# Kernel optimization log

Hardware: AMD Instinct MI355X
Metric: run time of the kernel (lower is better)

Reference implementation:

```python
import jax, jax.numpy as jnp
import numpy as np

N_NODES = 20000
N_EDGES = 640000
IN_DIM, HID_DIM, OUT_DIM = 128, 128, 64


def setup_inputs() -> dict:
    key = jax.random.key(0)
    k = jax.random.split(key, 6)
    x = jax.random.normal(k[0], (N_NODES, IN_DIM), dtype=jnp.float32)
    edge_index = jax.random.randint(k[1], (2, N_EDGES), 0, N_NODES, dtype=jnp.int64)
    W1 = jax.random.normal(k[2], (IN_DIM, HID_DIM), dtype=jnp.float32) * (1.0 / np.sqrt(IN_DIM))
    b1 = jnp.zeros((HID_DIM,), dtype=jnp.float32)
    W2 = jax.random.normal(k[3], (HID_DIM, OUT_DIM), dtype=jnp.float32) * (1.0 / np.sqrt(HID_DIM))
    b2 = jnp.zeros((OUT_DIM,), dtype=jnp.float32)
    return {"x": x, "edge_index": edge_index, "W1": W1, "b1": b1, "W2": W2, "b2": b2}


def _gcn_conv(h, W, b, src, dst, n_nodes):
    # h' = D^-1/2 (A + I) D^-1/2 (h W) + b   (PyG GCNConv with self-loops)
    h = h @ W                                              # [N, F_out]
    ones = jnp.ones((src.shape[0],), dtype=h.dtype)
    deg = jax.ops.segment_sum(ones, dst, num_segments=n_nodes) + 1.0  # +1 for self-loop
    dinv = jax.lax.rsqrt(deg)                              # [N]
    w = dinv[src] * dinv[dst]                              # per-edge norm [E]
    msg = h[src] * w[:, None]                              # gather + scale [E, F_out]
    agg = jax.ops.segment_sum(msg, dst, num_segments=n_nodes)  # scatter-add [N, F_out]
    # self-loop contribution: norm_ii = dinv[i]^2
    return agg + h * (dinv * dinv)[:, None] + b


def reference(x, edge_index, W1, b1, W2, b2):
    src, dst = edge_index[0], edge_index[1]
    n = x.shape[0]
    h = _gcn_conv(x, W1, b1, src, dst, n)
    h = jax.nn.relu(h)
    # dropout is identity in eval mode (training=False)
    out = _gcn_conv(h, W2, b2, src, dst, n)
    return out
```

## Files before the change

kernel.cpp:

```cpp
#include <hip/hip_runtime.h>


#define N_NODES 20000
#define N_EDGES 640000
#define IN_DIM 128
#define HID_DIM 128
#define OUT_DIM 64

#define STRIDE 80
#define NRANGE 8
#define RANGE_SZ (N_NODES / NRANGE)
#define SCAT_NB 2048
#define CHUNKS (SCAT_NB / NRANGE)
#define EPC (N_EDGES / CHUNKS)
#define G1_NB 625
#define G1_TASKS (2 * (N_NODES / 16))
#define PRE_ITEMS (128 * 128 + 64 * 128 + N_NODES)
#define PRE_NB ((PRE_ITEMS + 255) / 256)

typedef _Float16 half8_t __attribute__((ext_vector_type(8)));
typedef float float4_t __attribute__((ext_vector_type(4)));

__global__ __launch_bounds__(256) void k_pre(const float* __restrict__ W1,
                                             const float* __restrict__ W2,
                                             _Float16* __restrict__ WT1,
                                             _Float16* __restrict__ WT2,
                                             int* __restrict__ cnt) {
    int i = blockIdx.x * 256 + threadIdx.x;
    if (i < 128 * 128) {
        int c = i >> 7, k = i & 127;
        WT1[i] = (_Float16)W1[k * 128 + c];
    } else if (i < 128 * 128 + 64 * 128) {
        int o = i - 128 * 128;
        int c = o >> 7, k = o & 127;
        WT2[o] = (_Float16)W2[k * 64 + c];
    } else {
        int n = i - (128 * 128 + 64 * 128);
        if (n < N_NODES) cnt[n] = 0;
    }
}

__global__ __launch_bounds__(256) void k_front(const int* __restrict__ src,
                                               const int* __restrict__ dst,
                                               int* __restrict__ cnt,
                                               unsigned short* __restrict__ esrc_pad,
                                               const _Float16* __restrict__ WT1,
                                               const float* __restrict__ x,
                                               _Float16* __restrict__ GA,
                                               _Float16* __restrict__ GB) {
    const int b = blockIdx.x, tid = threadIdx.x;
    if (b < SCAT_NB) {
        const int g = b & 7;
        const int lo = g * RANGE_SZ;
        const int e0 = (b >> 3) * EPC;
        for (int i = tid; i < EPC; i += 256) {
            const int e = e0 + i;
            const int d = __builtin_nontemporal_load(&dst[e]);
            if ((unsigned int)(d - lo) < (unsigned int)RANGE_SZ) {
                const int s = __builtin_nontemporal_load(&src[e]);
                unsigned int rank = atomicAdd((unsigned int*)&cnt[d], 1u);
                if (rank < STRIDE) esrc_pad[d * STRIDE + rank] = (unsigned short)s;
            }
        }
        return;
    }
    const int wave = tid >> 6;
    const int lane = tid & 63;
    const int task = (b - SCAT_NB) * 4 + wave;
    if (task >= G1_TASKS) return;
    const int strip = task >> 1;
    const int nh = task & 1;
    const int row0 = strip * 16;
    const int mrow = row0 + (lane & 15);
    const int kq = (lane >> 4) * 8;
    _Float16* G = nh ? GB : GA;

    half8_t af[4];
#pragma unroll
    for (int kc = 0; kc < 4; ++kc) {
        const float* ap = x + (size_t)mrow * 128 + kc * 32 + kq;
        float4_t f0 = __builtin_nontemporal_load((const float4_t*)ap);
        float4_t f1 = __builtin_nontemporal_load((const float4_t*)(ap + 4));
        half8_t h;
        h[0] = (_Float16)f0[0]; h[1] = (_Float16)f0[1];
        h[2] = (_Float16)f0[2]; h[3] = (_Float16)f0[3];
        h[4] = (_Float16)f1[0]; h[5] = (_Float16)f1[1];
        h[6] = (_Float16)f1[2]; h[7] = (_Float16)f1[3];
        af[kc] = h;
    }
    float4_t acc[4];
#pragma unroll
    for (int nt = 0; nt < 4; ++nt) acc[nt] = (float4_t)(0.0f);
#pragma unroll
    for (int nt = 0; nt < 4; ++nt) {
        const _Float16* wp = WT1 + (size_t)((nh * 4 + nt) * 16 + (lane & 15)) * 128 + kq;
#pragma unroll
        for (int kc = 0; kc < 4; ++kc) {
            half8_t bf = *(const half8_t*)(wp + kc * 32);
            acc[nt] = __builtin_amdgcn_mfma_f32_16x16x32_f16(af[kc], bf, acc[nt], 0, 0, 0);
        }
    }
#pragma unroll
    for (int r = 0; r < 4; ++r) {
        int row = row0 + (lane >> 4) * 4 + r;
#pragma unroll
        for (int nt = 0; nt < 4; ++nt)
            G[(size_t)row * 64 + nt * 16 + (lane & 15)] = (_Float16)acc[nt][r];
    }
}

__global__ __launch_bounds__(256) void k_mid(const int* __restrict__ cnt,
                                             const unsigned short* __restrict__ esrc_pad,
                                             const _Float16* __restrict__ GA,
                                             const _Float16* __restrict__ GB,
                                             const _Float16* __restrict__ WT2,
                                             const float* __restrict__ b1,
                                             _Float16* __restrict__ g2) {
    __shared__ _Float16 h1[16][136];
    const int tid = threadIdx.x;
    const int wave = tid >> 6;
    const int lane = tid & 63;
    const int row0 = blockIdx.x * 16;
    const int eidx = lane >> 3;
    const int fl = lane & 7;

    for (int h = 0; h < 2; ++h) {
        const _Float16* __restrict__ G = h ? GB : GA;
        for (int r4 = 0; r4 < 4; ++r4) {
            const int rr = wave * 4 + r4;
            const int node = row0 + rr;
            const int endt = cnt[node];
            const float dvd = rsqrtf((float)endt + 1.0f);
            const int end = endt < STRIDE ? endt : STRIDE;
            const int base = node * STRIDE;

            float acc[8];
#pragma unroll
            for (int p = 0; p < 8; ++p) acc[p] = 0.0f;
            if (lane < 8) {
                half8_t sv = *(const half8_t*)(G + (size_t)node * 64 + fl * 8);
#pragma unroll
                for (int p = 0; p < 8; ++p) acc[p] = dvd * (float)sv[p];
            }
            int j = 0;
            for (; j + 15 < end; j += 16) {
                int s0 = (int)__builtin_nontemporal_load(&esrc_pad[base + j + eidx]);
                int s1 = (int)__builtin_nontemporal_load(&esrc_pad[base + j + 8 + eidx]);
                float dv0 = rsqrtf((float)cnt[s0] + 1.0f);
                float dv1 = rsqrtf((float)cnt[s1] + 1.0f);
                half8_t r0 = *(const half8_t*)(G + (size_t)s0 * 64 + fl * 8);
                half8_t r1 = *(const half8_t*)(G + (size_t)s1 * 64 + fl * 8);
#pragma unroll
                for (int p = 0; p < 8; ++p)
                    acc[p] += dv0 * (float)r0[p] + dv1 * (float)r1[p];
            }
            for (; j + 7 < end; j += 8) {
                int s = (int)__builtin_nontemporal_load(&esrc_pad[base + j + eidx]);
                float dvs = rsqrtf((float)cnt[s] + 1.0f);
                half8_t r = *(const half8_t*)(G + (size_t)s * 64 + fl * 8);
#pragma unroll
                for (int p = 0; p < 8; ++p) acc[p] += dvs * (float)r[p];
            }
            if (j < end) {
                int idx = j + eidx;
                int s = (int)__builtin_nontemporal_load(
                    &esrc_pad[base + ((idx < end) ? idx : (end - 1))]);
                float valid = (idx < end) ? 1.0f : 0.0f;
                float dvs = rsqrtf((float)cnt[s] + 1.0f);
                half8_t r = *(const half8_t*)(G + (size_t)s * 64 + fl * 8);
#pragma unroll
                for (int p = 0; p < 8; ++p) acc[p] += valid * dvs * (float)r[p];
            }
#pragma unroll
            for (int p = 0; p < 8; ++p) {
                acc[p] += __shfl_xor(acc[p], 32, 64);
                acc[p] += __shfl_xor(acc[p], 16, 64);
                acc[p] += __shfl_xor(acc[p], 8, 64);
            }
            if (lane < 8) {
                float4_t c0 = *(const float4_t*)(b1 + h * 64 + fl * 8);
                float4_t c1 = *(const float4_t*)(b1 + h * 64 + fl * 8 + 4);
                half8_t o;
                o[0] = (_Float16)fmaxf(acc[0] * dvd + c0[0], 0.0f);
                o[1] = (_Float16)fmaxf(acc[1] * dvd + c0[1], 0.0f);
                o[2] = (_Float16)fmaxf(acc[2] * dvd + c0[2], 0.0f);
                o[3] = (_Float16)fmaxf(acc[3] * dvd + c0[3], 0.0f);
                o[4] = (_Float16)fmaxf(acc[4] * dvd + c1[0], 0.0f);
                o[5] = (_Float16)fmaxf(acc[5] * dvd + c1[1], 0.0f);
                o[6] = (_Float16)fmaxf(acc[6] * dvd + c1[2], 0.0f);
                o[7] = (_Float16)fmaxf(acc[7] * dvd + c1[3], 0.0f);
                *(half8_t*)&h1[rr][h * 64 + fl * 8] = o;
            }
        }
    }
    __syncthreads();

    const int fr = lane & 15;
    const int kq = (lane >> 4) * 8;
    half8_t af[4];
#pragma unroll
    for (int kc = 0; kc < 4; ++kc)
        af[kc] = *(const half8_t*)&h1[fr][kc * 32 + kq];
    float4_t acc2 = (float4_t)(0.0f);
    const _Float16* wp = WT2 + (size_t)(wave * 16 + fr) * 128 + kq;
#pragma unroll
    for (int kc = 0; kc < 4; ++kc) {
        half8_t bf = *(const half8_t*)(wp + kc * 32);
        acc2 = __builtin_amdgcn_mfma_f32_16x16x32_f16(af[kc], bf, acc2, 0, 0, 0);
    }
#pragma unroll
    for (int r = 0; r < 4; ++r) {
        int row = row0 + (lane >> 4) * 4 + r;
        float dvr = rsqrtf((float)cnt[row] + 1.0f);
        g2[(size_t)row * 64 + wave * 16 + fr] = (_Float16)(dvr * acc2[r]);
    }
}

__global__ __launch_bounds__(256) void k_back(const int* __restrict__ cnt,
                                              const unsigned short* __restrict__ esrc_pad,
                                              const _Float16* __restrict__ g2,
                                              const float* __restrict__ b2,
                                              float* __restrict__ out) {
    const int wave = threadIdx.x >> 6;
    const int lane = threadIdx.x & 63;
    const int node = blockIdx.x * 4 + wave;
    if (node >= N_NODES) return;
    const int eidx = lane >> 3;
    const int fl = lane & 7;

    const int endt = cnt[node];
    const float dvd = rsqrtf((float)endt + 1.0f);
    const int end = endt < STRIDE ? endt : STRIDE;
    const int base = node * STRIDE;

    float acc[8];
#pragma unroll
    for (int p = 0; p < 8; ++p) acc[p] = 0.0f;
    if (lane < 8) {
        half8_t s = *(const half8_t*)(g2 + (size_t)node * 64 + fl * 8);
#pragma unroll
        for (int p = 0; p < 8; ++p) acc[p] = (float)s[p];
    }

    int j = 0;
    for (; j + 15 < end; j += 16) {
        int s0 = (int)__builtin_nontemporal_load(&esrc_pad[base + j + eidx]);
        int s1 = (int)__builtin_nontemporal_load(&esrc_pad[base + j + 8 + eidx]);
        half8_t r0 = *(const half8_t*)(g2 + (size_t)s0 * 64 + fl * 8);
        half8_t r1 = *(const half8_t*)(g2 + (size_t)s1 * 64 + fl * 8);
#pragma unroll
        for (int p = 0; p < 8; ++p) acc[p] += (float)r0[p] + (float)r1[p];
    }
    for (; j + 7 < end; j += 8) {
        int s = (int)__builtin_nontemporal_load(&esrc_pad[base + j + eidx]);
        half8_t r = *(const half8_t*)(g2 + (size_t)s * 64 + fl * 8);
#pragma unroll
        for (int p = 0; p < 8; ++p) acc[p] += (float)r[p];
    }
    if (j < end) {
        int idx = j + eidx;
        int s = (int)__builtin_nontemporal_load(
            &esrc_pad[base + ((idx < end) ? idx : (end - 1))]);
        float valid = (idx < end) ? 1.0f : 0.0f;
        half8_t r = *(const half8_t*)(g2 + (size_t)s * 64 + fl * 8);
#pragma unroll
        for (int p = 0; p < 8; ++p) acc[p] += valid * (float)r[p];
    }

#pragma unroll
    for (int p = 0; p < 8; ++p) {
        acc[p] += __shfl_xor(acc[p], 32, 64);
        acc[p] += __shfl_xor(acc[p], 16, 64);
        acc[p] += __shfl_xor(acc[p], 8, 64);
    }

    if (lane < 8) {
        float4_t c0 = *(const float4_t*)(b2 + fl * 8);
        float4_t c1 = *(const float4_t*)(b2 + fl * 8 + 4);
        float4_t o0, o1;
        o0[0] = acc[0] * dvd + c0[0]; o0[1] = acc[1] * dvd + c0[1];
        o0[2] = acc[2] * dvd + c0[2]; o0[3] = acc[3] * dvd + c0[3];
        o1[0] = acc[4] * dvd + c1[0]; o1[1] = acc[5] * dvd + c1[1];
        o1[2] = acc[6] * dvd + c1[2]; o1[3] = acc[7] * dvd + c1[3];
        __builtin_nontemporal_store(o0, (float4_t*)(out + (size_t)node * 64 + fl * 8));
        __builtin_nontemporal_store(o1, (float4_t*)(out + (size_t)node * 64 + fl * 8 + 4));
    }
}

extern "C" void kernel_launch(void* const* d_in, const int* in_sizes, int n_in,
                              void* d_out, int out_size, void* d_ws, size_t ws_size,
                              hipStream_t stream) {
    const float* x  = (const float*)d_in[0];
    const int*   ei = (const int*)d_in[1];
    const float* W1 = (const float*)d_in[2];
    const float* b1 = (const float*)d_in[3];
    const float* W2 = (const float*)d_in[4];
    const float* b2 = (const float*)d_in[5];

    const int* src = ei;
    const int* dst = ei + N_EDGES;

    char* w = (char*)d_ws;
    unsigned short* esrc_pad = (unsigned short*)w; w += sizeof(unsigned short) * (size_t)N_NODES * STRIDE;
    _Float16*       GA       = (_Float16*)w;       w += sizeof(_Float16) * (size_t)N_NODES * 64;
    _Float16*       GB       = (_Float16*)w;       w += sizeof(_Float16) * (size_t)N_NODES * 64;
    _Float16*       g2       = (_Float16*)w;       w += sizeof(_Float16) * (size_t)N_NODES * OUT_DIM;
    _Float16*       WT1      = (_Float16*)w;       w += sizeof(_Float16) * 128 * 128;
    _Float16*       WT2      = (_Float16*)w;       w += sizeof(_Float16) * 64 * 128;
    int*            cnt      = (int*)w;            w += sizeof(int) * N_NODES;
    float*          out      = (float*)d_out;

    k_pre<<<PRE_NB, 256, 0, stream>>>(W1, W2, WT1, WT2, cnt);
    k_front<<<SCAT_NB + G1_NB, 256, 0, stream>>>(src, dst, cnt, esrc_pad, WT1, x, GA, GB);
    k_mid<<<N_NODES / 16, 256, 0, stream>>>(cnt, esrc_pad, GA, GB, WT2, b1, g2);
    k_back<<<(N_NODES + 3) / 4, 256, 0, stream>>>(cnt, esrc_pad, g2, b2, out);
}
```

Baseline: 178.6 us.

## Bucket edges in shared memory per node range and fuse both halves in mid gather

Edge bucketing no longer uses global atomics. Destinations are first compacted to 16-bit, then each of 160 blocks scans every edge and builds its node range's adjacency lists and counts with LDS atomics before copying them out with coalesced writes. The mid kernel now processes the GA and GB halves together, so each edge list and degree is read once, and the gather loops in mid and back are unrolled to 32 edges. The trade-off is that every scatter block reads the whole edge array, which adds redundant bandwidth and puts the bucketing on only 160 blocks. The wider unroll also raises register pressure.

After: 392.0 us. +119.5%, slower.

```diff
diff --git a/kernel.cpp b/kernel.cpp
--- a/kernel.cpp
+++ b/kernel.cpp
@@ -8,25 +8,23 @@
 #define OUT_DIM 64
 
 #define STRIDE 80
-#define NRANGE 8
-#define RANGE_SZ (N_NODES / NRANGE)
-#define SCAT_NB 2048
-#define CHUNKS (SCAT_NB / NRANGE)
-#define EPC (N_EDGES / CHUNKS)
+#define SC_NB 160
+#define NODES_PB (N_NODES / SC_NB)
 #define G1_NB 625
 #define G1_TASKS (2 * (N_NODES / 16))
-#define PRE_ITEMS (128 * 128 + 64 * 128 + N_NODES)
-#define PRE_NB ((PRE_ITEMS + 255) / 256)
+#define PRE_NB 176
 
 typedef _Float16 half8_t __attribute__((ext_vector_type(8)));
 typedef float float4_t __attribute__((ext_vector_type(4)));
+typedef unsigned short ushort8_t __attribute__((ext_vector_type(8)));
 
 __global__ __launch_bounds__(256) void k_pre(const float* __restrict__ W1,
                                              const float* __restrict__ W2,
                                              _Float16* __restrict__ WT1,
                                              _Float16* __restrict__ WT2,
-                                             int* __restrict__ cnt) {
-    int i = blockIdx.x * 256 + threadIdx.x;
+                                             const int* __restrict__ dst,
+                                             unsigned short* __restrict__ dst16) {
+    const int i = blockIdx.x * 256 + threadIdx.x;
     if (i < 128 * 128) {
         int c = i >> 7, k = i & 127;
         WT1[i] = (_Float16)W1[k * 128 + c];
@@ -34,39 +32,50 @@
         int o = i - 128 * 128;
         int c = o >> 7, k = o & 127;
         WT2[o] = (_Float16)W2[k * 64 + c];
-    } else {
-        int n = i - (128 * 128 + 64 * 128);
-        if (n < N_NODES) cnt[n] = 0;
-    }
+    }
+    for (int e = i; e < N_EDGES; e += PRE_NB * 256)
+        dst16[e] = (unsigned short)dst[e];
 }
 
 __global__ __launch_bounds__(256) void k_front(const int* __restrict__ src,
-                                               const int* __restrict__ dst,
+                                               const unsigned short* __restrict__ dst16,
                                                int* __restrict__ cnt,
                                                unsigned short* __restrict__ esrc_pad,
                                                const _Float16* __restrict__ WT1,
                                                const float* __restrict__ x,
                                                _Float16* __restrict__ GA,
                                                _Float16* __restrict__ GB) {
+    __shared__ unsigned short lbuck[NODES_PB * STRIDE];
+    __shared__ int lhist[NODES_PB];
     const int b = blockIdx.x, tid = threadIdx.x;
-    if (b < SCAT_NB) {
-        const int g = b & 7;
-        const int lo = g * RANGE_SZ;
-        const int e0 = (b >> 3) * EPC;
-        for (int i = tid; i < EPC; i += 256) {
-            const int e = e0 + i;
-            const int d = __builtin_nontemporal_load(&dst[e]);
-            if ((unsigned int)(d - lo) < (unsigned int)RANGE_SZ) {
-                const int s = __builtin_nontemporal_load(&src[e]);
-                unsigned int rank = atomicAdd((unsigned int*)&cnt[d], 1u);
-                if (rank < STRIDE) esrc_pad[d * STRIDE + rank] = (unsigned short)s;
-            }
-        }
+    if (b < SC_NB) {
+        for (int i = tid; i < NODES_PB; i += 256) lhist[i] = 0;
+        __syncthreads();
+        const unsigned int lo = b * NODES_PB;
+        const ushort8_t* d8 = (const ushort8_t*)dst16;
+        for (int i = tid; i < N_EDGES / 8; i += 256) {
+            ushort8_t dv = d8[i];
+            const int e0 = i * 8;
+#pragma unroll
+            for (int q = 0; q < 8; ++q) {
+                unsigned int ln = (unsigned int)dv[q] - lo;
+                if (ln < (unsigned int)NODES_PB) {
+                    int s = src[e0 + q];
+                    int r = atomicAdd(&lhist[ln], 1);
+                    if (r < STRIDE) lbuck[ln * STRIDE + r] = (unsigned short)s;
+                }
+            }
+        }
+        __syncthreads();
+        for (int i = tid; i < NODES_PB; i += 256) cnt[lo + i] = lhist[i];
+        const unsigned int* ls = (const unsigned int*)lbuck;
+        unsigned int* gd = (unsigned int*)(esrc_pad + (size_t)lo * STRIDE);
+        for (int i = tid; i < NODES_PB * STRIDE / 2; i += 256) gd[i] = ls[i];
         return;
     }
     const int wave = tid >> 6;
     const int lane = tid & 63;
-    const int task = (b - SCAT_NB) * 4 + wave;
+    const int task = (b - SC_NB) * 4 + wave;
     if (task >= G1_TASKS) return;
     const int strip = task >> 1;
     const int nh = task & 1;
@@ -124,73 +133,124 @@
     const int eidx = lane >> 3;
     const int fl = lane & 7;
 
-    for (int h = 0; h < 2; ++h) {
-        const _Float16* __restrict__ G = h ? GB : GA;
-        for (int r4 = 0; r4 < 4; ++r4) {
-            const int rr = wave * 4 + r4;
-            const int node = row0 + rr;
-            const int endt = cnt[node];
-            const float dvd = rsqrtf((float)endt + 1.0f);
-            const int end = endt < STRIDE ? endt : STRIDE;
-            const int base = node * STRIDE;
-
-            float acc[8];
-#pragma unroll
-            for (int p = 0; p < 8; ++p) acc[p] = 0.0f;
-            if (lane < 8) {
-                half8_t sv = *(const half8_t*)(G + (size_t)node * 64 + fl * 8);
-#pragma unroll
-                for (int p = 0; p < 8; ++p) acc[p] = dvd * (float)sv[p];
-            }
-            int j = 0;
-            for (; j + 15 < end; j += 16) {
-                int s0 = (int)__builtin_nontemporal_load(&esrc_pad[base + j + eidx]);
-                int s1 = (int)__builtin_nontemporal_load(&esrc_pad[base + j + 8 + eidx]);
-                float dv0 = rsqrtf((float)cnt[s0] + 1.0f);
-                float dv1 = rsqrtf((float)cnt[s1] + 1.0f);
-                half8_t r0 = *(const half8_t*)(G + (size_t)s0 * 64 + fl * 8);
-                half8_t r1 = *(const half8_t*)(G + (size_t)s1 * 64 + fl * 8);
-#pragma unroll
-                for (int p = 0; p < 8; ++p)
-                    acc[p] += dv0 * (float)r0[p] + dv1 * (float)r1[p];
-            }
-            for (; j + 7 < end; j += 8) {
-                int s = (int)__builtin_nontemporal_load(&esrc_pad[base + j + eidx]);
-                float dvs = rsqrtf((float)cnt[s] + 1.0f);
-                half8_t r = *(const half8_t*)(G + (size_t)s * 64 + fl * 8);
-#pragma unroll
-                for (int p = 0; p < 8; ++p) acc[p] += dvs * (float)r[p];
-            }
-            if (j < end) {
-                int idx = j + eidx;
-                int s = (int)__builtin_nontemporal_load(
-                    &esrc_pad[base + ((idx < end) ? idx : (end - 1))]);
-                float valid = (idx < end) ? 1.0f : 0.0f;
-                float dvs = rsqrtf((float)cnt[s] + 1.0f);
-                half8_t r = *(const half8_t*)(G + (size_t)s * 64 + fl * 8);
-#pragma unroll
-                for (int p = 0; p < 8; ++p) acc[p] += valid * dvs * (float)r[p];
-            }
-#pragma unroll
-            for (int p = 0; p < 8; ++p) {
-                acc[p] += __shfl_xor(acc[p], 32, 64);
-                acc[p] += __shfl_xor(acc[p], 16, 64);
-                acc[p] += __shfl_xor(acc[p], 8, 64);
-            }
-            if (lane < 8) {
-                float4_t c0 = *(const float4_t*)(b1 + h * 64 + fl * 8);
-                float4_t c1 = *(const float4_t*)(b1 + h * 64 + fl * 8 + 4);
-                half8_t o;
-                o[0] = (_Float16)fmaxf(acc[0] * dvd + c0[0], 0.0f);
-                o[1] = (_Float16)fmaxf(acc[1] * dvd + c0[1], 0.0f);
-                o[2] = (_Float16)fmaxf(acc[2] * dvd + c0[2], 0.0f);
-                o[3] = (_Float16)fmaxf(acc[3] * dvd + c0[3], 0.0f);
-                o[4] = (_Float16)fmaxf(acc[4] * dvd + c1[0], 0.0f);
-                o[5] = (_Float16)fmaxf(acc[5] * dvd + c1[1], 0.0f);
-                o[6] = (_Float16)fmaxf(acc[6] * dvd + c1[2], 0.0f);
-                o[7] = (_Float16)fmaxf(acc[7] * dvd + c1[3], 0.0f);
-                *(half8_t*)&h1[rr][h * 64 + fl * 8] = o;
-            }
+    for (int r4 = 0; r4 < 4; ++r4) {
+        const int rr = wave * 4 + r4;
+        const int node = row0 + rr;
+        const int endt = cnt[node];
+        const float dvd = rsqrtf((float)endt + 1.0f);
+        const int end = endt < STRIDE ? endt : STRIDE;
+        const int base = node * STRIDE;
+
+        float accA[8], accB[8];
+#pragma unroll
+        for (int p = 0; p < 8; ++p) { accA[p] = 0.0f; accB[p] = 0.0f; }
+        if (lane < 8) {
+            half8_t sa = *(const half8_t*)(GA + (size_t)node * 64 + fl * 8);
+            half8_t sb = *(const half8_t*)(GB + (size_t)node * 64 + fl * 8);
+#pragma unroll
+            for (int p = 0; p < 8; ++p) {
+                accA[p] = dvd * (float)sa[p];
+                accB[p] = dvd * (float)sb[p];
+            }
+        }
+        int j = 0;
+        for (; j + 31 < end; j += 32) {
+            int s0 = (int)esrc_pad[base + j + eidx];
+            int s1 = (int)esrc_pad[base + j + 8 + eidx];
+            int s2 = (int)esrc_pad[base + j + 16 + eidx];
+            int s3 = (int)esrc_pad[base + j + 24 + eidx];
+            float d0 = rsqrtf((float)cnt[s0] + 1.0f);
+            float d1 = rsqrtf((float)cnt[s1] + 1.0f);
+            float d2 = rsqrtf((float)cnt[s2] + 1.0f);
+            float d3 = rsqrtf((float)cnt[s3] + 1.0f);
+            half8_t a0 = *(const half8_t*)(GA + (size_t)s0 * 64 + fl * 8);
+            half8_t a1 = *(const half8_t*)(GA + (size_t)s1 * 64 + fl * 8);
+            half8_t a2 = *(const half8_t*)(GA + (size_t)s2 * 64 + fl * 8);
+            half8_t a3 = *(const half8_t*)(GA + (size_t)s3 * 64 + fl * 8);
+            half8_t v0 = *(const half8_t*)(GB + (size_t)s0 * 64 + fl * 8);
+            half8_t v1 = *(const half8_t*)(GB + (size_t)s1 * 64 + fl * 8);
+            half8_t v2 = *(const half8_t*)(GB + (size_t)s2 * 64 + fl * 8);
+            half8_t v3 = *(const half8_t*)(GB + (size_t)s3 * 64 + fl * 8);
+#pragma unroll
+            for (int p = 0; p < 8; ++p) {
+                accA[p] += d0 * (float)a0[p] + d1 * (float)a1[p] +
+                           d2 * (float)a2[p] + d3 * (float)a3[p];
+                accB[p] += d0 * (float)v0[p] + d1 * (float)v1[p] +
+                           d2 * (float)v2[p] + d3 * (float)v3[p];
+            }
+        }
+        for (; j + 15 < end; j += 16) {
+            int s0 = (int)esrc_pad[base + j + eidx];
+            int s1 = (int)esrc_pad[base + j + 8 + eidx];
+            float d0 = rsqrtf((float)cnt[s0] + 1.0f);
+            float d1 = rsqrtf((float)cnt[s1] + 1.0f);
+            half8_t a0 = *(const half8_t*)(GA + (size_t)s0 * 64 + fl * 8);
+            half8_t a1 = *(const half8_t*)(GA + (size_t)s1 * 64 + fl * 8);
+            half8_t v0 = *(const half8_t*)(GB + (size_t)s0 * 64 + fl * 8);
+            half8_t v1 = *(const half8_t*)(GB + (size_t)s1 * 64 + fl * 8);
+#pragma unroll
+            for (int p = 0; p < 8; ++p) {
+                accA[p] += d0 * (float)a0[p] + d1 * (float)a1[p];
+                accB[p] += d0 * (float)v0[p] + d1 * (float)v1[p];
+            }
+        }
+        for (; j + 7 < end; j += 8) {
+            int s = (int)esrc_pad[base + j + eidx];
+            float dv = rsqrtf((float)cnt[s] + 1.0f);
+            half8_t a = *(const half8_t*)(GA + (size_t)s * 64 + fl * 8);
+            half8_t v = *(const half8_t*)(GB + (size_t)s * 64 + fl * 8);
+#pragma unroll
+            for (int p = 0; p < 8; ++p) {
+                accA[p] += dv * (float)a[p];
+                accB[p] += dv * (float)v[p];
+            }
+        }
+        if (j < end) {
+            int idx = j + eidx;
+            int s = (int)esrc_pad[base + ((idx < end) ? idx : (end - 1))];
+            float valid = (idx < end) ? 1.0f : 0.0f;
+            float dv = valid * rsqrtf((float)cnt[s] + 1.0f);
+            half8_t a = *(const half8_t*)(GA + (size_t)s * 64 + fl * 8);
+            half8_t v = *(const half8_t*)(GB + (size_t)s * 64 + fl * 8);
+#pragma unroll
+            for (int p = 0; p < 8; ++p) {
+                accA[p] += dv * (float)a[p];
+                accB[p] += dv * (float)v[p];
+            }
+        }
+#pragma unroll
+        for (int p = 0; p < 8; ++p) {
+            accA[p] += __shfl_xor(accA[p], 8, 64);
+            accA[p] += __shfl_xor(accA[p], 16, 64);
+            accA[p] += __shfl_xor(accA[p], 32, 64);
+            accB[p] += __shfl_xor(accB[p], 8, 64);
+            accB[p] += __shfl_xor(accB[p], 16, 64);
+            accB[p] += __shfl_xor(accB[p], 32, 64);
+        }
+        if (lane < 8) {
+            float4_t c0 = *(const float4_t*)(b1 + fl * 8);
+            float4_t c1 = *(const float4_t*)(b1 + fl * 8 + 4);
+            float4_t c2 = *(const float4_t*)(b1 + 64 + fl * 8);
+            float4_t c3 = *(const float4_t*)(b1 + 64 + fl * 8 + 4);
+            half8_t oa, ob;
+            oa[0] = (_Float16)fmaxf(accA[0] * dvd + c0[0], 0.0f);
+            oa[1] = (_Float16)fmaxf(accA[1] * dvd + c0[1], 0.0f);
+            oa[2] = (_Float16)fmaxf(accA[2] * dvd + c0[2], 0.0f);
+            oa[3] = (_Float16)fmaxf(accA[3] * dvd + c0[3], 0.0f);
+            oa[4] = (_Float16)fmaxf(accA[4] * dvd + c1[0], 0.0f);
+            oa[5] = (_Float16)fmaxf(accA[5] * dvd + c1[1], 0.0f);
+            oa[6] = (_Float16)fmaxf(accA[6] * dvd + c1[2], 0.0f);
+            oa[7] = (_Float16)fmaxf(accA[7] * dvd + c1[3], 0.0f);
+            ob[0] = (_Float16)fmaxf(accB[0] * dvd + c2[0], 0.0f);
+            ob[1] = (_Float16)fmaxf(accB[1] * dvd + c2[1], 0.0f);
+            ob[2] = (_Float16)fmaxf(accB[2] * dvd + c2[2], 0.0f);
+            ob[3] = (_Float16)fmaxf(accB[3] * dvd + c2[3], 0.0f);
+            ob[4] = (_Float16)fmaxf(accB[4] * dvd + c3[0], 0.0f);
+            ob[5] = (_Float16)fmaxf(accB[5] * dvd + c3[1], 0.0f);
+            ob[6] = (_Float16)fmaxf(accB[6] * dvd + c3[2], 0.0f);
+            ob[7] = (_Float16)fmaxf(accB[7] * dvd + c3[3], 0.0f);
+            *(half8_t*)&h1[rr][fl * 8] = oa;
+            *(half8_t*)&h1[rr][64 + fl * 8] = ob;
         }
     }
     __syncthreads();
@@ -243,24 +303,36 @@
     }
 
     int j = 0;
-    for (; j + 15 < end; j += 16) {
-        int s0 = (int)__builtin_nontemporal_load(&esrc_pad[base + j + eidx]);
-        int s1 = (int)__builtin_nontemporal_load(&esrc_pad[base + j + 8 + eidx]);
+    for (; j + 31 < end; j += 32) {
+        int s0 = (int)esrc_pad[base + j + eidx];
+        int s1 = (int)esrc_pad[base + j + 8 + eidx];
+        int s2 = (int)esrc_pad[base + j + 16 + eidx];
+        int s3 = (int)esrc_pad[base + j + 24 + eidx];
         half8_t r0 = *(const half8_t*)(g2 + (size_t)s0 * 64 + fl * 8);
         half8_t r1 = *(const half8_t*)(g2 + (size_t)s1 * 64 + fl * 8);
+        half8_t r2 = *(const half8_t*)(g2 + (size_t)s2 * 64 + fl * 8);
+        half8_t r3 = *(const half8_t*)(g2 + (size_t)s3 * 64 + fl * 8);
+#pragma unroll
+        for (int p = 0; p < 8; ++p)
+            acc[p] += ((float)r0[p] + (float)r1[p]) + ((float)r2[p] + (float)r3[p]);
+    }
+    for (; j + 15 < end; j += 16) {
+        int s0 = (int)esrc_pad[base + j + eidx];
+        int s1 = (int)esrc_pad[base + j + 8 + eidx];
+        half8_t r0 = *(const half8_t*)(g2 + (size_t)s0 * 64 + fl * 8);
+        half8_t r1 = *(const half8_t*)(g2 + (size_t)s1 * 64 + fl * 8);
 #pragma unroll
         for (int p = 0; p < 8; ++p) acc[p] += (float)r0[p] + (float)r1[p];
     }
     for (; j + 7 < end; j += 8) {
-        int s = (int)__builtin_nontemporal_load(&esrc_pad[base + j + eidx]);
+        int s = (int)esrc_pad[base + j + eidx];
         half8_t r = *(const half8_t*)(g2 + (size_t)s * 64 + fl * 8);
 #pragma unroll
         for (int p = 0; p < 8; ++p) acc[p] += (float)r[p];
     }
     if (j < end) {
         int idx = j + eidx;
-        int s = (int)__builtin_nontemporal_load(
-            &esrc_pad[base + ((idx < end) ? idx : (end - 1))]);
+        int s = (int)esrc_pad[base + ((idx < end) ? idx : (end - 1))];
         float valid = (idx < end) ? 1.0f : 0.0f;
         half8_t r = *(const half8_t*)(g2 + (size_t)s * 64 + fl * 8);
 #pragma unroll
@@ -269,9 +341,9 @@
 
 #pragma unroll
     for (int p = 0; p < 8; ++p) {
+        acc[p] += __shfl_xor(acc[p], 8, 64);
+        acc[p] += __shfl_xor(acc[p], 16, 64);
         acc[p] += __shfl_xor(acc[p], 32, 64);
-        acc[p] += __shfl_xor(acc[p], 16, 64);
-        acc[p] += __shfl_xor(acc[p], 8, 64);
     }
 
     if (lane < 8) {
@@ -302,6 +374,7 @@
 
     char* w = (char*)d_ws;
     unsigned short* esrc_pad = (unsigned short*)w; w += sizeof(unsigned short) * (size_t)N_NODES * STRIDE;
+    unsigned short* dst16    = (unsigned short*)w; w += sizeof(unsigned short) * (size_t)N_EDGES;
     _Float16*       GA       = (_Float16*)w;       w += sizeof(_Float16) * (size_t)N_NODES * 64;
     _Float16*       GB       = (_Float16*)w;       w += sizeof(_Float16) * (size_t)N_NODES * 64;
     _Float16*       g2       = (_Float16*)w;       w += sizeof(_Float16) * (size_t)N_NODES * OUT_DIM;
@@ -310,8 +383,8 @@
     int*            cnt      = (int*)w;            w += sizeof(int) * N_NODES;
     float*          out      = (float*)d_out;
 
-    k_pre<<<PRE_NB, 256, 0, stream>>>(W1, W2, WT1, WT2, cnt);
-    k_front<<<SCAT_NB + G1_NB, 256, 0, stream>>>(src, dst, cnt, esrc_pad, WT1, x, GA, GB);
+    k_pre<<<PRE_NB, 256, 0, stream>>>(W1, W2, WT1, WT2, dst, dst16);
+    k_front<<<SC_NB + G1_NB, 256, 0, stream>>>(src, dst16, cnt, esrc_pad, WT1, x, GA, GB);
     k_mid<<<N_NODES / 16, 256, 0, stream>>>(cnt, esrc_pad, GA, GB, WT2, b1, g2);
     k_back<<<(N_NODES + 3) / 4, 256, 0, stream>>>(cnt, esrc_pad, g2, b2, out);
 }
```

## Split mid stage into aggregation and GEMM kernels, flatten edge scatter, batch gathers

Applied to the files above, without the earlier changes.

The edge bucketing no longer scans all edges once per destination range; each thread handles one edge with a single atomic. The fused layer-1 aggregation plus layer-2 GEMM kernel is split into a per-node aggregation kernel that writes h1 to global memory, followed by a separate MFMA GEMM kernel. Both aggregation kernels now issue the first 64 neighbor gathers up front, masking and clamping indices so the loads can be in flight together. This buys more parallelism and memory-level overlap at the cost of an extra launch and an h1 round trip through global memory. The up-front gathers also read unfilled padding slots, and that depends on the clamp being correct.

Result: faster. 164.9 us (-7.7%).

```diff
diff --git a/kernel.cpp b/kernel.cpp
--- a/kernel.cpp
+++ b/kernel.cpp
@@ -8,15 +8,12 @@
 #define OUT_DIM 64
 
 #define STRIDE 80
-#define NRANGE 8
-#define RANGE_SZ (N_NODES / NRANGE)
-#define SCAT_NB 2048
-#define CHUNKS (SCAT_NB / NRANGE)
-#define EPC (N_EDGES / CHUNKS)
+#define SCAT_NB (N_EDGES / 256)
 #define G1_NB 625
 #define G1_TASKS (2 * (N_NODES / 16))
 #define PRE_ITEMS (128 * 128 + 64 * 128 + N_NODES)
 #define PRE_NB ((PRE_ITEMS + 255) / 256)
+#define AGG_NB (N_NODES / 4)
 
 typedef _Float16 half8_t __attribute__((ext_vector_type(8)));
 typedef float float4_t __attribute__((ext_vector_type(4)));
@@ -40,7 +37,7 @@
     }
 }
 
-__global__ __launch_bounds__(256) void k_front(const int* __restrict__ src,
+__global__ __launch_bounds__(256) void k_build(const int* __restrict__ src,
                                                const int* __restrict__ dst,
                                                int* __restrict__ cnt,
                                                unsigned short* __restrict__ esrc_pad,
@@ -50,18 +47,11 @@
                                                _Float16* __restrict__ GB) {
     const int b = blockIdx.x, tid = threadIdx.x;
     if (b < SCAT_NB) {
-        const int g = b & 7;
-        const int lo = g * RANGE_SZ;
-        const int e0 = (b >> 3) * EPC;
-        for (int i = tid; i < EPC; i += 256) {
-            const int e = e0 + i;
-            const int d = __builtin_nontemporal_load(&dst[e]);
-            if ((unsigned int)(d - lo) < (unsigned int)RANGE_SZ) {
-                const int s = __builtin_nontemporal_load(&src[e]);
-                unsigned int rank = atomicAdd((unsigned int*)&cnt[d], 1u);
-                if (rank < STRIDE) esrc_pad[d * STRIDE + rank] = (unsigned short)s;
-            }
-        }
+        const int e = b * 256 + tid;
+        const int s = __builtin_nontemporal_load(&src[e]);
+        const int d = __builtin_nontemporal_load(&dst[e]);
+        unsigned int rank = atomicAdd((unsigned int*)&cnt[d], 1u);
+        if (rank < STRIDE) esrc_pad[d * STRIDE + rank] = (unsigned short)s;
         return;
     }
     const int wave = tid >> 6;
@@ -109,114 +99,134 @@
     }
 }
 
-__global__ __launch_bounds__(256) void k_mid(const int* __restrict__ cnt,
-                                             const unsigned short* __restrict__ esrc_pad,
-                                             const _Float16* __restrict__ GA,
-                                             const _Float16* __restrict__ GB,
-                                             const _Float16* __restrict__ WT2,
-                                             const float* __restrict__ b1,
-                                             _Float16* __restrict__ g2) {
-    __shared__ _Float16 h1[16][136];
-    const int tid = threadIdx.x;
-    const int wave = tid >> 6;
-    const int lane = tid & 63;
-    const int row0 = blockIdx.x * 16;
+__global__ __launch_bounds__(256) void k_agg1(const int* __restrict__ cnt,
+                                              const unsigned short* __restrict__ esrc_pad,
+                                              const _Float16* __restrict__ GA,
+                                              const _Float16* __restrict__ GB,
+                                              const float* __restrict__ b1,
+                                              _Float16* __restrict__ h1p) {
+    const int half = (blockIdx.x >= AGG_NB) ? 1 : 0;
+    const int bb = blockIdx.x - half * AGG_NB;
+    const int wave = threadIdx.x >> 6;
+    const int lane = threadIdx.x & 63;
+    const int node = bb * 4 + wave;
+    const _Float16* __restrict__ G = half ? GB : GA;
+    const int COL0 = half << 6;
     const int eidx = lane >> 3;
     const int fl = lane & 7;
 
-    for (int h = 0; h < 2; ++h) {
-        const _Float16* __restrict__ G = h ? GB : GA;
-        for (int r4 = 0; r4 < 4; ++r4) {
-            const int rr = wave * 4 + r4;
-            const int node = row0 + rr;
-            const int endt = cnt[node];
-            const float dvd = rsqrtf((float)endt + 1.0f);
-            const int end = endt < STRIDE ? endt : STRIDE;
-            const int base = node * STRIDE;
-
-            float acc[8];
-#pragma unroll
-            for (int p = 0; p < 8; ++p) acc[p] = 0.0f;
-            if (lane < 8) {
-                half8_t sv = *(const half8_t*)(G + (size_t)node * 64 + fl * 8);
-#pragma unroll
-                for (int p = 0; p < 8; ++p) acc[p] = dvd * (float)sv[p];
-            }
-            int j = 0;
-            for (; j + 15 < end; j += 16) {
-                int s0 = (int)__builtin_nontemporal_load(&esrc_pad[base + j + eidx]);
-                int s1 = (int)__builtin_nontemporal_load(&esrc_pad[base + j + 8 + eidx]);
-                float dv0 = rsqrtf((float)cnt[s0] + 1.0f);
-                float dv1 = rsqrtf((float)cnt[s1] + 1.0f);
-                half8_t r0 = *(const half8_t*)(G + (size_t)s0 * 64 + fl * 8);
-                half8_t r1 = *(const half8_t*)(G + (size_t)s1 * 64 + fl * 8);
-#pragma unroll
-                for (int p = 0; p < 8; ++p)
-                    acc[p] += dv0 * (float)r0[p] + dv1 * (float)r1[p];
-            }
-            for (; j + 7 < end; j += 8) {
-                int s = (int)__builtin_nontemporal_load(&esrc_pad[base + j + eidx]);
-                float dvs = rsqrtf((float)cnt[s] + 1.0f);
-                half8_t r = *(const half8_t*)(G + (size_t)s * 64 + fl * 8);
-#pragma unroll
-                for (int p = 0; p < 8; ++p) acc[p] += dvs * (float)r[p];
-            }
-            if (j < end) {
-                int idx = j + eidx;
-                int s = (int)__builtin_nontemporal_load(
-                    &esrc_pad[base + ((idx < end) ? idx : (end - 1))]);
-                float valid = (idx < end) ? 1.0f : 0.0f;
-                float dvs = rsqrtf((float)cnt[s] + 1.0f);
-                half8_t r = *(const half8_t*)(G + (size_t)s * 64 + fl * 8);
-#pragma unroll
-                for (int p = 0; p < 8; ++p) acc[p] += valid * dvs * (float)r[p];
-            }
-#pragma unroll
-            for (int p = 0; p < 8; ++p) {
-                acc[p] += __shfl_xor(acc[p], 32, 64);
-                acc[p] += __shfl_xor(acc[p], 16, 64);
-                acc[p] += __shfl_xor(acc[p], 8, 64);
-            }
-            if (lane < 8) {
-                float4_t c0 = *(const float4_t*)(b1 + h * 64 + fl * 8);
-                float4_t c1 = *(const float4_t*)(b1 + h * 64 + fl * 8 + 4);
-                half8_t o;
-                o[0] = (_Float16)fmaxf(acc[0] * dvd + c0[0], 0.0f);
-                o[1] = (_Float16)fmaxf(acc[1] * dvd + c0[1], 0.0f);
-                o[2] = (_Float16)fmaxf(acc[2] * dvd + c0[2], 0.0f);
-                o[3] = (_Float16)fmaxf(acc[3] * dvd + c0[3], 0.0f);
-                o[4] = (_Float16)fmaxf(acc[4] * dvd + c1[0], 0.0f);
-                o[5] = (_Float16)fmaxf(acc[5] * dvd + c1[1], 0.0f);
-                o[6] = (_Float16)fmaxf(acc[6] * dvd + c1[2], 0.0f);
-                o[7] = (_Float16)fmaxf(acc[7] * dvd + c1[3], 0.0f);
-                *(half8_t*)&h1[rr][h * 64 + fl * 8] = o;
-            }
+    const int endt = cnt[node];
+    const float dvd = rsqrtf((float)endt + 1.0f);
+    const int end = endt < STRIDE ? endt : STRIDE;
+    const int base = node * STRIDE;
+
+    int sv[8];
+#pragma unroll
+    for (int k = 0; k < 8; ++k) {
+        int raw = (int)esrc_pad[base + 8 * k + eidx];
+        sv[k] = raw < N_NODES ? raw : (N_NODES - 1);
+    }
+    float dvs[8];
+#pragma unroll
+    for (int k = 0; k < 8; ++k) {
+        float valid = (8 * k + eidx < end) ? 1.0f : 0.0f;
+        dvs[k] = valid * rsqrtf((float)cnt[sv[k]] + 1.0f);
+    }
+    half8_t rv[8];
+#pragma unroll
+    for (int k = 0; k < 8; ++k)
+        rv[k] = *(const half8_t*)(G + (size_t)sv[k] * 64 + fl * 8);
+
+    float acc[8];
+#pragma unroll
+    for (int p = 0; p < 8; ++p) acc[p] = 0.0f;
+    if (lane < 8) {
+        half8_t s = *(const half8_t*)(G + (size_t)node * 64 + fl * 8);
+#pragma unroll
+        for (int p = 0; p < 8; ++p) acc[p] = dvd * (float)s[p];
+    }
+#pragma unroll
+    for (int k = 0; k < 8; ++k)
+#pragma unroll
+        for (int p = 0; p < 8; ++p) acc[p] += dvs[k] * (float)rv[k][p];
+
+    for (int j = 64; j < end; j += 8) {
+        int idx = j + eidx;
+        int s = (int)esrc_pad[base + ((idx < end) ? idx : (end - 1))];
+        float valid = (idx < end) ? 1.0f : 0.0f;
+        float dv = valid * rsqrtf((float)cnt[s] + 1.0f);
+        half8_t r = *(const half8_t*)(G + (size_t)s * 64 + fl * 8);
+#pragma unroll
+        for (int p = 0; p < 8; ++p) acc[p] += dv * (float)r[p];
+    }
+
+#pragma unroll
+    for (int p = 0; p < 8; ++p) {
+        acc[p] += __shfl_xor(acc[p], 8, 64);
+        acc[p] += __shfl_xor(acc[p], 16, 64);
+        acc[p] += __shfl_xor(acc[p], 32, 64);
+    }
+
+    if (lane < 8) {
+        float4_t c0 = *(const float4_t*)(b1 + COL0 + fl * 8);
+        float4_t c1 = *(const float4_t*)(b1 + COL0 + fl * 8 + 4);
+        half8_t o;
+        o[0] = (_Float16)fmaxf(acc[0] * dvd + c0[0], 0.0f);
+        o[1] = (_Float16)fmaxf(acc[1] * dvd + c0[1], 0.0f);
+        o[2] = (_Float16)fmaxf(acc[2] * dvd + c0[2], 0.0f);
+        o[3] = (_Float16)fmaxf(acc[3] * dvd + c0[3], 0.0f);
+        o[4] = (_Float16)fmaxf(acc[4] * dvd + c1[0], 0.0f);
+        o[5] = (_Float16)fmaxf(acc[5] * dvd + c1[1], 0.0f);
+        o[6] = (_Float16)fmaxf(acc[6] * dvd + c1[2], 0.0f);
+        o[7] = (_Float16)fmaxf(acc[7] * dvd + c1[3], 0.0f);
+        *(half8_t*)(h1p + (size_t)node * 128 + COL0 + fl * 8) = o;
+    }
+}
+
+__global__ __launch_bounds__(256) void k_g2(const _Float16* __restrict__ A,
+                                            const _Float16* __restrict__ WT,
+                                            const int* __restrict__ cnt,
+                                            _Float16* __restrict__ G) {
+    const int wave = threadIdx.x >> 6;
+    const int lane = threadIdx.x & 63;
+    const int task = blockIdx.x * 4 + wave;
+    if (task >= G1_TASKS) return;
+    const int strip = task >> 1;
+    const int nh = task & 1;
+    const int row0 = strip * 16;
+    const int mrow = row0 + (lane & 15);
+    const int kq = (lane >> 4) * 8;
+
+    half8_t af[4];
+#pragma unroll
+    for (int kc = 0; kc < 4; ++kc)
+        af[kc] = __builtin_nontemporal_load(
+            (const half8_t*)(A + (size_t)mrow * 128 + kc * 32 + kq));
+
+    float4_t acc[2];
+#pragma unroll
+    for (int nt = 0; nt < 2; ++nt) acc[nt] = (float4_t)(0.0f);
+#pragma unroll
+    for (int nt = 0; nt < 2; ++nt) {
+        const _Float16* wp = WT + (size_t)((nh * 2 + nt) * 16 + (lane & 15)) * 128 + kq;
+#pragma unroll
+        for (int kc = 0; kc < 4; ++kc) {
+            half8_t bf = *(const half8_t*)(wp + kc * 32);
+            acc[nt] = __builtin_amdgcn_mfma_f32_16x16x32_f16(af[kc], bf, acc[nt], 0, 0, 0);
         }
-    }
-    __syncthreads();
-
-    const int fr = lane & 15;
-    const int kq = (lane >> 4) * 8;
-    half8_t af[4];
-#pragma unroll
-    for (int kc = 0; kc < 4; ++kc)
-        af[kc] = *(const half8_t*)&h1[fr][kc * 32 + kq];
-    float4_t acc2 = (float4_t)(0.0f);
-    const _Float16* wp = WT2 + (size_t)(wave * 16 + fr) * 128 + kq;
-#pragma unroll
-    for (int kc = 0; kc < 4; ++kc) {
-        half8_t bf = *(const half8_t*)(wp + kc * 32);
-        acc2 = __builtin_amdgcn_mfma_f32_16x16x32_f16(af[kc], bf, acc2, 0, 0, 0);
     }
 #pragma unroll
     for (int r = 0; r < 4; ++r) {
         int row = row0 + (lane >> 4) * 4 + r;
         float dvr = rsqrtf((float)cnt[row] + 1.0f);
-        g2[(size_t)row * 64 + wave * 16 + fr] = (_Float16)(dvr * acc2[r]);
-    }
-}
-
-__global__ __launch_bounds__(256) void k_back(const int* __restrict__ cnt,
+#pragma unroll
+        for (int nt = 0; nt < 2; ++nt)
+            G[(size_t)row * 64 + (nh * 2 + nt) * 16 + (lane & 15)] =
+                (_Float16)(dvr * acc[nt][r]);
+    }
+}
+
+__global__ __launch_bounds__(256) void k_agg2(const int* __restrict__ cnt,
                                               const unsigned short* __restrict__ esrc_pad,
                                               const _Float16* __restrict__ g2,
                                               const float* __restrict__ b2,
@@ -224,7 +234,6 @@
     const int wave = threadIdx.x >> 6;
     const int lane = threadIdx.x & 63;
     const int node = blockIdx.x * 4 + wave;
-    if (node >= N_NODES) return;
     const int eidx = lane >> 3;
     const int fl = lane & 7;
 
@@ -233,6 +242,21 @@
     const int end = endt < STRIDE ? endt : STRIDE;
     const int base = node * STRIDE;
 
+    int sv[8];
+#pragma unroll
+    for (int k = 0; k < 8; ++k) {
+        int raw = (int)esrc_pad[base + 8 * k + eidx];
+        sv[k] = raw < N_NODES ? raw : (N_NODES - 1);
+    }
+    float vm[8];
+#pragma unroll
+    for (int k = 0; k < 8; ++k)
+        vm[k] = (8 * k + eidx < end) ? 1.0f : 0.0f;
+    half8_t rv[8];
+#pragma unroll
+    for (int k = 0; k < 8; ++k)
+        rv[k] = *(const half8_t*)(g2 + (size_t)sv[k] * 64 + fl * 8);
+
     float acc[8];
 #pragma unroll
     for (int p = 0; p < 8; ++p) acc[p] = 0.0f;
@@ -241,26 +265,14 @@
 #pragma unroll
         for (int p = 0; p < 8; ++p) acc[p] = (float)s[p];
     }
-
-    int j = 0;
-    for (; j + 15 < end; j += 16) {
-        int s0 = (int)__builtin_nontemporal_load(&esrc_pad[base + j + eidx]);
-        int s1 = (int)__builtin_nontemporal_load(&esrc_pad[base + j + 8 + eidx]);
-        half8_t r0 = *(const half8_t*)(g2 + (size_t)s0 * 64 + fl * 8);
-        half8_t r1 = *(const half8_t*)(g2 + (size_t)s1 * 64 + fl * 8);
-#pragma unroll
-        for (int p = 0; p < 8; ++p) acc[p] += (float)r0[p] + (float)r1[p];
-    }
-    for (; j + 7 < end; j += 8) {
-        int s = (int)__builtin_nontemporal_load(&esrc_pad[base + j + eidx]);
-        half8_t r = *(const half8_t*)(g2 + (size_t)s * 64 + fl * 8);
-#pragma unroll
-        for (int p = 0; p < 8; ++p) acc[p] += (float)r[p];
-    }
-    if (j < end) {
+#pragma unroll
+    for (int k = 0; k < 8; ++k)
+#pragma unroll
+        for (int p = 0; p < 8; ++p) acc[p] += vm[k] * (float)rv[k][p];
+
+    for (int j = 64; j < end; j += 8) {
         int idx = j + eidx;
-        int s = (int)__builtin_nontemporal_load(
-            &esrc_pad[base + ((idx < end) ? idx : (end - 1))]);
+        int s = (int)esrc_pad[base + ((idx < end) ? idx : (end - 1))];
         float valid = (idx < end) ? 1.0f : 0.0f;
         half8_t r = *(const half8_t*)(g2 + (size_t)s * 64 + fl * 8);
 #pragma unroll
@@ -269,9 +281,9 @@
 
 #pragma unroll
     for (int p = 0; p < 8; ++p) {
+        acc[p] += __shfl_xor(acc[p], 8, 64);
+        acc[p] += __shfl_xor(acc[p], 16, 64);
         acc[p] += __shfl_xor(acc[p], 32, 64);
-        acc[p] += __shfl_xor(acc[p], 16, 64);
-        acc[p] += __shfl_xor(acc[p], 8, 64);
     }
 
     if (lane < 8) {
@@ -304,6 +316,7 @@
     unsigned short* esrc_pad = (unsigned short*)w; w += sizeof(unsigned short) * (size_t)N_NODES * STRIDE;
     _Float16*       GA       = (_Float16*)w;       w += sizeof(_Float16) * (size_t)N_NODES * 64;
     _Float16*       GB       = (_Float16*)w;       w += sizeof(_Float16) * (size_t)N_NODES * 64;
+    _Float16*       h1p      = (_Float16*)w;       w += sizeof(_Float16) * (size_t)N_NODES * HID_DIM;
     _Float16*       g2       = (_Float16*)w;       w += sizeof(_Float16) * (size_t)N_NODES * OUT_DIM;
     _Float16*       WT1      = (_Float16*)w;       w += sizeof(_Float16) * 128 * 128;
     _Float16*       WT2      = (_Float16*)w;       w += sizeof(_Float16) * 64 * 128;
@@ -311,7 +324,8 @@
     float*          out      = (float*)d_out;
 
     k_pre<<<PRE_NB, 256, 0, stream>>>(W1, W2, WT1, WT2, cnt);
-    k_front<<<SCAT_NB + G1_NB, 256, 0, stream>>>(src, dst, cnt, esrc_pad, WT1, x, GA, GB);
-    k_mid<<<N_NODES / 16, 256, 0, stream>>>(cnt, esrc_pad, GA, GB, WT2, b1, g2);
-    k_back<<<(N_NODES + 3) / 4, 256, 0, stream>>>(cnt, esrc_pad, g2, b2, out);
-}
+    k_build<<<SCAT_NB + G1_NB, 256, 0, stream>>>(src, dst, cnt, esrc_pad, WT1, x, GA, GB);
+    k_agg1<<<2 * AGG_NB, 256, 0, stream>>>(cnt, esrc_pad, GA, GB, b1, h1p);
+    k_g2<<<G1_NB, 256, 0, stream>>>(h1p, WT2, cnt, g2);
+    k_agg2<<<AGG_NB, 256, 0, stream>>>(cnt, esrc_pad, g2, b2, out);
+}
```
